# Performance work log

Measured on AMD Instinct MI355X. Metric: run time of the kernel, lower is better.

## Reference

```python
import jax, jax.numpy as jnp
import numpy as np

N_EMBD = 1024

def setup_inputs() -> dict:
    key = jax.random.key(0)
    ks = jax.random.split(key, 7)
    x = jax.random.normal(ks[0], (4, 2048, N_EMBD), dtype=jnp.float32)
    s = 1.0 / np.sqrt(N_EMBD)
    Wk = jax.random.normal(ks[1], (N_EMBD, N_EMBD), dtype=jnp.float32) * s
    bk = jnp.zeros((N_EMBD,), dtype=jnp.float32)
    Wq = jax.random.normal(ks[2], (N_EMBD, N_EMBD), dtype=jnp.float32) * s
    bq = jnp.zeros((N_EMBD,), dtype=jnp.float32)
    Wv = jax.random.normal(ks[3], (N_EMBD, N_EMBD), dtype=jnp.float32) * s
    bv = jnp.zeros((N_EMBD,), dtype=jnp.float32)
    return {"x": x, "Wk": Wk, "bk": bk, "Wq": Wq, "bq": bq, "Wv": Wv, "bv": bv}

def reference(x, Wk, bk, Wq, bq, Wv, bv):
    B, T, C = x.shape
    k = x @ Wk.T + bk  # [B,T,C]
    q = x @ Wq.T + bq
    v = x @ Wv.T + bv
    # scaled scores with causal mask (note: original scales by C**-0.5)
    scores = jnp.einsum('btc,bsc->bts', q, k) * (C ** -0.5)  # [B,T,T]
    causal = jnp.tril(jnp.ones((T, T), dtype=bool))
    scores = jnp.where(causal, scores, -jnp.inf)
    weights = jax.nn.softmax(scores, axis=-1)
    # dropout disabled (inference mode)
    y = jnp.einsum('bts,bsc->btc', weights, v)
    return y
```

## Files before the change

kernel.cpp:

```cpp
#include <hip/hip_runtime.h>
#include <hip/hip_bf16.h>

typedef __attribute__((ext_vector_type(8))) short short8;
typedef __attribute__((ext_vector_type(4))) float f32x4;

__device__ __forceinline__ ushort f2b(float f) {
    __hip_bfloat16 h = __float2bfloat16(f);
    return *reinterpret_cast<ushort*>(&h);
}
__device__ __forceinline__ float b2f(ushort u) {
    return __uint_as_float(((unsigned)u) << 16);
}
__device__ __forceinline__ void gload16(const ushort* g, ushort* l) {
    __builtin_amdgcn_global_load_lds(
        (const __attribute__((address_space(1))) void*)g,
        (__attribute__((address_space(3))) void*)l, 16, 0, 0);
}

__global__ __launch_bounds__(512, 4) void qkv_gemm256(
    const ushort* __restrict__ xb, const ushort* __restrict__ Wcat,
    const float* __restrict__ bk, const float* __restrict__ bq, const float* __restrict__ bv,
    ushort* __restrict__ Kb, ushort* __restrict__ Qb, ushort* __restrict__ Vt) {
    constexpr int T = 2048, C = 1024, K = 1024, NT = 32;
    __shared__ ushort smem[36864];

    const int tid = threadIdx.x;
    const int l = tid & 63, w = tid >> 6;
    const int wm = (w >> 1) * 64, wn = (w & 1) * 64;
    const int lr = l & 15, lk = l >> 4;

    const int b = blockIdx.x;
    const int wg = (b & 7) * 96 + (b >> 3);
    const int m0 = (wg / 24) * 256, n0 = (wg % 24) * 128;

    const int srow = w * 16 + (l >> 2);
    const int scb = ((l & 3) << 4) ^ ((l & 32) ? 32 : 0);
    const ushort* gA = xb + (size_t)(m0 + srow) * K + (scb >> 1);
    const ushort* gB = Wcat + (size_t)(n0 + srow) * K + (scb >> 1);

    const int LB = lr * 32 + ((lk << 3) ^ ((lr >= 8) ? 16 : 0));

    f32x4 acc[4][4] = {};

#define STAGEQ(tt, sl)                                                    \
    {                                                                     \
        const int _ko = (tt) * 32;                                        \
        ushort* _s = smem + (sl) * 12288 + w * 512;                       \
        gload16(gA + _ko,                   _s);                          \
        gload16(gA + (size_t)128 * K + _ko, _s + 4096);                   \
        gload16(gB + _ko,                   _s + 8192);                   \
    }

    STAGEQ(0, 0);
    STAGEQ(1, 1);
    asm volatile("s_waitcnt vmcnt(3)" ::: "memory");
    __builtin_amdgcn_s_barrier();
    asm volatile("" ::: "memory");

    int sc = 0, ss = 2;
    for (int t = 0; t < NT; ++t) {
        const ushort* slot = smem + sc * 12288;
        const ushort* Ab = slot + (wm >> 4) * 512 + LB;
        const ushort* Bb = slot + 8192 + (wn >> 4) * 512 + LB;
        short8 af[4], bf4[4];
#pragma unroll
        for (int f = 0; f < 4; ++f) af[f] = *reinterpret_cast<const short8*>(Ab + f * 512);
#pragma unroll
        for (int g = 0; g < 4; ++g) bf4[g] = *reinterpret_cast<const short8*>(Bb + g * 512);
        if (t + 2 < NT) STAGEQ(t + 2, ss);
        __builtin_amdgcn_s_setprio(1);
#pragma unroll
        for (int f = 0; f < 4; ++f)
#pragma unroll
            for (int g = 0; g < 4; ++g)
                acc[f][g] = __builtin_amdgcn_mfma_f32_16x16x32_bf16(af[f], bf4[g], acc[f][g], 0, 0, 0);
        __builtin_amdgcn_s_setprio(0);
        if (t + 1 < NT) {
            if (t + 2 < NT) asm volatile("s_waitcnt vmcnt(3)" ::: "memory");
            else            asm volatile("s_waitcnt vmcnt(0)" ::: "memory");
            __builtin_amdgcn_s_barrier();
            asm volatile("" ::: "memory");
        }
        sc = (sc == 2) ? 0 : sc + 1;
        ss = (ss == 2) ? 0 : ss + 1;
    }
#undef STAGEQ

    const int zsel = n0 >> 10;
    const int c0 = (n0 & 1023) + wn;
    if (zsel < 2) {
        ushort* O = (zsel == 0) ? Kb : Qb;
        const float* bias = (zsel == 0) ? bk : bq;
#pragma unroll
        for (int f = 0; f < 4; ++f)
#pragma unroll
            for (int g = 0; g < 4; ++g) {
                const int gc = c0 + g * 16 + lr;
                const float badd = bias[gc];
#pragma unroll
                for (int rr = 0; rr < 4; ++rr) {
                    const int gr = m0 + wm + f * 16 + lk * 4 + rr;
                    O[(size_t)gr * C + gc] = f2b(acc[f][g][rr] + badd);
                }
            }
    } else {
        const int zb = (m0 + wm) >> 11;
        const int s0 = (m0 + wm) & 2047;
        ushort* Vz = Vt + (size_t)zb * C * T;
#pragma unroll
        for (int f = 0; f < 4; ++f)
#pragma unroll
            for (int g = 0; g < 4; ++g) {
                const int gc = c0 + g * 16 + lr;
                const float badd = bv[gc];
                const int s = s0 + f * 16 + lk * 4;
                ushort tmp[4];
#pragma unroll
                for (int rr = 0; rr < 4; ++rr) tmp[rr] = f2b(acc[f][g][rr] + badd);
                *reinterpret_cast<uint2*>(Vz + (size_t)gc * T + s) =
                    *reinterpret_cast<uint2*>(tmp);
            }
    }
}

template <int MODE>
__global__ __launch_bounds__(256, 3) void gemm_ring(
    const ushort* __restrict__ Kb, const ushort* __restrict__ Qb,
    const ushort* __restrict__ Vt, ushort* __restrict__ Sb, float* __restrict__ out) {
    constexpr int T = 2048, C = 1024;
    __shared__ ushort smem[24576];

    const int tid = threadIdx.x;
    const int l = tid & 63, w = tid >> 6;
    const int wm = (w >> 1) * 64, wn = (w & 1) * 64;
    const int lr = l & 15, lk = l >> 4;

    int m0, n0, nt, iblk = 0, jblk = 0, z = 0;
    const ushort *Au, *Bu;
    int ldA, ldB;
    if constexpr (MODE == 1) {
        const int wg0 = blockIdx.x;
        const int wg = (wg0 & 7) * 68 + (wg0 >> 3);
        z = wg / 136; const int t136 = wg % 136;
        int i = (int)((sqrtf(8.f * t136 + 1.f) - 1.f) * 0.5f);
        while ((i + 1) * (i + 2) / 2 <= t136) ++i;
        while (i * (i + 1) / 2 > t136) --i;
        const int j = t136 - i * (i + 1) / 2;
        iblk = i; jblk = j;
        m0 = i * 128; n0 = j * 128;
        Au = Qb + (size_t)z * T * C + (size_t)m0 * C; ldA = C;
        Bu = Kb + (size_t)z * T * C + (size_t)n0 * C; ldB = C;
        nt = 32;
    } else {
        const int wg0 = blockIdx.x;
        const int wg = (wg0 & 7) * 64 + (wg0 >> 3);
        const int half = wg >> 8, s2 = wg & 255;
        z = s2 >> 6; const int r6 = s2 & 63;
        const int nb = r6 & 7, ii = r6 >> 3;
        const int i = half ? (15 - ii) : ii;
        iblk = i;
        m0 = i * 128; n0 = nb * 128;
        Au = Sb + (size_t)z * T * T + (size_t)m0 * T; ldA = T;
        Bu = Vt + (size_t)z * C * T + (size_t)n0 * T; ldB = T;
        nt = 4 * (i + 1);
    }

    const int srow = w * 16 + (l >> 2);
    const int scb = ((l & 3) << 4) ^ ((l >= 32) ? 32 : 0);
    const ushort* gA = Au + (size_t)srow * ldA + (scb >> 1);
    const ushort* gB = Bu + (size_t)srow * ldB + (scb >> 1);
    const size_t a64 = (size_t)64 * ldA, b64 = (size_t)64 * ldB;
    const int LBu = lr * 32 + ((lk << 3) ^ ((lr >= 8) ? 16 : 0));

    f32x4 acc[4][4] = {};
    f32x4 acc1[4] = {};
    short8 ones;
#pragma unroll
    for (int q = 0; q < 8; ++q) ones[q] = (short)0x3F80;

#define STAGE(tt, sl)                                                    \
    {                                                                    \
        const int _ko = (tt) * 32;                                       \
        ushort* _d = smem + (sl) * 8192 + w * 512;                       \
        gload16(gA + _ko,        _d);                                    \
        gload16(gA + a64 + _ko,  _d + 2048);                             \
        gload16(gB + _ko,        _d + 4096);                             \
        gload16(gB + b64 + _ko,  _d + 6144);                             \
    }

    STAGE(0, 0);
    STAGE(1, 1);
    asm volatile("s_waitcnt vmcnt(4)" ::: "memory");
    __builtin_amdgcn_s_barrier();
    asm volatile("" ::: "memory");

    int sc = 0, ss = 2;
    for (int t = 0; t < nt; ++t) {
        const ushort* As = smem + sc * 8192 + (wm >> 4) * 512 + LBu;
        const ushort* Bs = smem + sc * 8192 + 4096 + (wn >> 4) * 512 + LBu;
        short8 af[4], bf[4];
#pragma unroll
        for (int q = 0; q < 4; ++q) {
            af[q] = *reinterpret_cast<const short8*>(As + q * 512);
            bf[q] = *reinterpret_cast<const short8*>(Bs + q * 512);
        }
        if (t + 2 < nt) STAGE(t + 2, ss);
        __builtin_amdgcn_s_setprio(1);
#pragma unroll
        for (int mf = 0; mf < 4; ++mf)
#pragma unroll
            for (int nf = 0; nf < 4; ++nf)
                acc[mf][nf] = __builtin_amdgcn_mfma_f32_16x16x32_bf16(af[mf], bf[nf], acc[mf][nf], 0, 0, 0);
        if constexpr (MODE == 2) {
#pragma unroll
            for (int mf = 0; mf < 4; ++mf)
                acc1[mf] = __builtin_amdgcn_mfma_f32_16x16x32_bf16(af[mf], ones, acc1[mf], 0, 0, 0);
        }
        __builtin_amdgcn_s_setprio(0);
        if (t + 1 < nt) {
            if (t + 2 < nt) asm volatile("s_waitcnt vmcnt(4)" ::: "memory");
            else            asm volatile("s_waitcnt vmcnt(0)" ::: "memory");
            __builtin_amdgcn_s_barrier();
            asm volatile("" ::: "memory");
        }
        sc = (sc == 2) ? 0 : sc + 1;
        ss = (ss == 2) ? 0 : ss + 1;
    }
#undef STAGE

    if constexpr (MODE == 1) {
        ushort* Sp = Sb + (size_t)z * T * T;
        const bool diag = (iblk == jblk);
#pragma unroll
        for (int mf = 0; mf < 4; ++mf)
#pragma unroll
            for (int nf = 0; nf < 4; ++nf) {
                const int gc = n0 + wn + nf * 16 + lr;
#pragma unroll
                for (int rr = 0; rr < 4; ++rr) {
                    const int gr = m0 + wm + mf * 16 + lk * 4 + rr;
                    float p = __expf(acc[mf][nf][rr] * 0.03125f);
                    if (diag && gc > gr) p = 0.f;
                    Sp[(size_t)gr * T + gc] = f2b(p);
                }
            }
    } else {
        float* Op = out + (size_t)z * T * C;
#pragma unroll
        for (int mf = 0; mf < 4; ++mf)
#pragma unroll
            for (int rr = 0; rr < 4; ++rr) {
                const int gr = m0 + wm + mf * 16 + lk * 4 + rr;
                const float inv = 1.0f / acc1[mf][rr];
#pragma unroll
                for (int nf = 0; nf < 4; ++nf) {
                    const int gc = n0 + wn + nf * 16 + lr;
                    Op[(size_t)gr * C + gc] = acc[mf][nf][rr] * inv;
                }
            }
    }
}

__global__ __launch_bounds__(256) void cvt_all(
    const float* __restrict__ x, const float* __restrict__ Wk,
    const float* __restrict__ Wq, const float* __restrict__ Wv,
    ushort* __restrict__ xb, ushort* __restrict__ Wcat) {
    constexpr int C = 1024;
    constexpr int NX = 8388608 / 8, NW = C * C / 8;
    int i = blockIdx.x * 256 + threadIdx.x;
    const float* src; ushort* dst;
    if (i < NX)               { src = x;  dst = xb; }
    else if (i < NX + NW)     { src = Wk; dst = Wcat;                 i -= NX; }
    else if (i < NX + 2 * NW) { src = Wq; dst = Wcat + (size_t)C * C; i -= NX + NW; }
    else                      { src = Wv; dst = Wcat + 2 * (size_t)C * C; i -= NX + 2 * NW; }
    const float4* p = reinterpret_cast<const float4*>(src) + (size_t)i * 2;
    float4 a = p[0], b = p[1];
    ushort o[8] = {f2b(a.x), f2b(a.y), f2b(a.z), f2b(a.w),
                   f2b(b.x), f2b(b.y), f2b(b.z), f2b(b.w)};
    reinterpret_cast<uint4*>(dst)[i] = *reinterpret_cast<uint4*>(o);
}

extern "C" void kernel_launch(void* const* d_in, const int* in_sizes, int n_in,
                              void* d_out, int out_size, void* d_ws, size_t ws_size,
                              hipStream_t stream) {
    const float* x  = (const float*)d_in[0];
    const float* Wk = (const float*)d_in[1];
    const float* bk = (const float*)d_in[2];
    const float* Wq = (const float*)d_in[3];
    const float* bq = (const float*)d_in[4];
    const float* Wv = (const float*)d_in[5];
    const float* bv = (const float*)d_in[6];
    float* out = (float*)d_out;

    constexpr int B = 4, T = 2048, C = 1024;
    constexpr size_t BTC = (size_t)B * T * C;

    ushort* Kb = (ushort*)d_ws;
    ushort* Qb = Kb + BTC;
    ushort* Vt = Qb + BTC;
    ushort* Sb = Vt + BTC;
    ushort* xb   = Sb;
    ushort* Wcat = Sb + BTC;

    dim3 blk(256);

    cvt_all<<<dim3(5632), blk, 0, stream>>>(x, Wk, Wq, Wv, xb, Wcat);

    qkv_gemm256<<<dim3(768), dim3(512), 0, stream>>>(xb, Wcat, bk, bq, bv, Kb, Qb, Vt);

    gemm_ring<1><<<dim3(544), blk, 0, stream>>>(Kb, Qb, Vt, Sb, out);

    gemm_ring<2><<<dim3(512), blk, 0, stream>>>(Kb, Qb, Vt, Sb, out);
}
```

Before: 136.8 us.

## Retile QKV GEMM to 128x192 blocks and compute softmax row sums via atomics

The QKV projection GEMM moves from 256x128 tiles on 768 blocks to 128x192 tiles on 1024 blocks, with 8 waves laid out 2x4 at 64x48 each. The epilogue now chooses the K/Q/V destination per 16-column fragment, because a 192-wide tile can straddle the K/Q/V boundaries. Separately, the PV GEMM no longer spends extra MFMAs against a ones vector to get softmax denominators. Instead the score kernel sums the rounded bf16 probabilities per row, reduces them with wave shuffles, and atomically adds them into a rowsum buffer that the conversion kernel zeroes. This adds float atomics and extra workspace, and the load balance changes across the retiled blocks.

```diff
diff --git a/kernel.cpp b/kernel.cpp
--- a/kernel.cpp
+++ b/kernel.cpp
@@ -17,66 +17,72 @@
         (__attribute__((address_space(3))) void*)l, 16, 0, 0);
 }
 
-__global__ __launch_bounds__(512, 4) void qkv_gemm256(
+__global__ __launch_bounds__(512, 4) void qkv_gemm(
     const ushort* __restrict__ xb, const ushort* __restrict__ Wcat,
     const float* __restrict__ bk, const float* __restrict__ bq, const float* __restrict__ bv,
     ushort* __restrict__ Kb, ushort* __restrict__ Qb, ushort* __restrict__ Vt) {
     constexpr int T = 2048, C = 1024, K = 1024, NT = 32;
-    __shared__ ushort smem[36864];
+    __shared__ ushort smem[30720];
 
     const int tid = threadIdx.x;
     const int l = tid & 63, w = tid >> 6;
-    const int wm = (w >> 1) * 64, wn = (w & 1) * 64;
+    const int wm = (w >> 2) * 64, wn = (w & 3) * 48;
     const int lr = l & 15, lk = l >> 4;
 
     const int b = blockIdx.x;
-    const int wg = (b & 7) * 96 + (b >> 3);
-    const int m0 = (wg / 24) * 256, n0 = (wg % 24) * 128;
+    const int wg = (b & 7) * 128 + (b >> 3);
+    const int m0 = (wg >> 4) * 128, n0 = (wg & 15) * 192;
 
     const int srow = w * 16 + (l >> 2);
     const int scb = ((l & 3) << 4) ^ ((l & 32) ? 32 : 0);
-    const ushort* gA = xb + (size_t)(m0 + srow) * K + (scb >> 1);
-    const ushort* gB = Wcat + (size_t)(n0 + srow) * K + (scb >> 1);
+    const ushort* gA  = xb + (size_t)(m0 + srow) * K + (scb >> 1);
+    const ushort* gB  = Wcat + (size_t)(n0 + srow) * K + (scb >> 1);
+    const ushort* gB2 = Wcat + (size_t)(n0 + 128 + srow) * K + (scb >> 1);
 
     const int LB = lr * 32 + ((lk << 3) ^ ((lr >= 8) ? 16 : 0));
 
-    f32x4 acc[4][4] = {};
+    f32x4 acc[4][3] = {};
 
 #define STAGEQ(tt, sl)                                                    \
     {                                                                     \
         const int _ko = (tt) * 32;                                        \
-        ushort* _s = smem + (sl) * 12288 + w * 512;                       \
-        gload16(gA + _ko,                   _s);                          \
-        gload16(gA + (size_t)128 * K + _ko, _s + 4096);                   \
-        gload16(gB + _ko,                   _s + 8192);                   \
+        ushort* _s = smem + (sl) * 10240;                                 \
+        gload16(gA + _ko,  _s + w * 512);                                 \
+        gload16(gB + _ko,  _s + 4096 + w * 512);                          \
+        if (w < 4) gload16(gB2 + _ko, _s + 8192 + w * 512);               \
+    }
+#define WAIT_KEEP1                                                        \
+    {                                                                     \
+        if (w < 4) asm volatile("s_waitcnt vmcnt(3)" ::: "memory");       \
+        else       asm volatile("s_waitcnt vmcnt(2)" ::: "memory");       \
     }
 
     STAGEQ(0, 0);
     STAGEQ(1, 1);
-    asm volatile("s_waitcnt vmcnt(3)" ::: "memory");
+    WAIT_KEEP1;
     __builtin_amdgcn_s_barrier();
     asm volatile("" ::: "memory");
 
     int sc = 0, ss = 2;
     for (int t = 0; t < NT; ++t) {
-        const ushort* slot = smem + sc * 12288;
+        const ushort* slot = smem + sc * 10240;
         const ushort* Ab = slot + (wm >> 4) * 512 + LB;
-        const ushort* Bb = slot + 8192 + (wn >> 4) * 512 + LB;
-        short8 af[4], bf4[4];
+        const ushort* Bb = slot + 4096 + (wn >> 4) * 512 + LB;
+        short8 af[4], bf3[3];
 #pragma unroll
         for (int f = 0; f < 4; ++f) af[f] = *reinterpret_cast<const short8*>(Ab + f * 512);
 #pragma unroll
-        for (int g = 0; g < 4; ++g) bf4[g] = *reinterpret_cast<const short8*>(Bb + g * 512);
+        for (int g = 0; g < 3; ++g) bf3[g] = *reinterpret_cast<const short8*>(Bb + g * 512);
         if (t + 2 < NT) STAGEQ(t + 2, ss);
         __builtin_amdgcn_s_setprio(1);
 #pragma unroll
         for (int f = 0; f < 4; ++f)
 #pragma unroll
-            for (int g = 0; g < 4; ++g)
-                acc[f][g] = __builtin_amdgcn_mfma_f32_16x16x32_bf16(af[f], bf4[g], acc[f][g], 0, 0, 0);
+            for (int g = 0; g < 3; ++g)
+                acc[f][g] = __builtin_amdgcn_mfma_f32_16x16x32_bf16(af[f], bf3[g], acc[f][g], 0, 0, 0);
         __builtin_amdgcn_s_setprio(0);
         if (t + 1 < NT) {
-            if (t + 2 < NT) asm volatile("s_waitcnt vmcnt(3)" ::: "memory");
+            if (t + 2 < NT) { WAIT_KEEP1; }
             else            asm volatile("s_waitcnt vmcnt(0)" ::: "memory");
             __builtin_amdgcn_s_barrier();
             asm volatile("" ::: "memory");
@@ -85,48 +91,46 @@
         ss = (ss == 2) ? 0 : ss + 1;
     }
 #undef STAGEQ
-
-    const int zsel = n0 >> 10;
-    const int c0 = (n0 & 1023) + wn;
-    if (zsel < 2) {
-        ushort* O = (zsel == 0) ? Kb : Qb;
-        const float* bias = (zsel == 0) ? bk : bq;
-#pragma unroll
-        for (int f = 0; f < 4; ++f)
-#pragma unroll
-            for (int g = 0; g < 4; ++g) {
-                const int gc = c0 + g * 16 + lr;
-                const float badd = bias[gc];
+#undef WAIT_KEEP1
+
+    const int zb = (m0 + wm) >> 11;
+    const int s0 = (m0 + wm) & 2047;
+    ushort* Vz = Vt + (size_t)zb * C * T;
+#pragma unroll
+    for (int g = 0; g < 3; ++g) {
+        const int nbase = n0 + wn + g * 16;
+        const int zf = nbase >> 10;
+        const int cf = (nbase & 1023) + lr;
+        if (zf < 2) {
+            ushort* O = (zf == 0) ? Kb : Qb;
+            const float badd = ((zf == 0) ? bk : bq)[cf];
+#pragma unroll
+            for (int f = 0; f < 4; ++f)
 #pragma unroll
                 for (int rr = 0; rr < 4; ++rr) {
                     const int gr = m0 + wm + f * 16 + lk * 4 + rr;
-                    O[(size_t)gr * C + gc] = f2b(acc[f][g][rr] + badd);
+                    O[(size_t)gr * C + cf] = f2b(acc[f][g][rr] + badd);
                 }
-            }
-    } else {
-        const int zb = (m0 + wm) >> 11;
-        const int s0 = (m0 + wm) & 2047;
-        ushort* Vz = Vt + (size_t)zb * C * T;
-#pragma unroll
-        for (int f = 0; f < 4; ++f)
-#pragma unroll
-            for (int g = 0; g < 4; ++g) {
-                const int gc = c0 + g * 16 + lr;
-                const float badd = bv[gc];
+        } else {
+            const float badd = bv[cf];
+#pragma unroll
+            for (int f = 0; f < 4; ++f) {
                 const int s = s0 + f * 16 + lk * 4;
                 ushort tmp[4];
 #pragma unroll
                 for (int rr = 0; rr < 4; ++rr) tmp[rr] = f2b(acc[f][g][rr] + badd);
-                *reinterpret_cast<uint2*>(Vz + (size_t)gc * T + s) =
+                *reinterpret_cast<uint2*>(Vz + (size_t)cf * T + s) =
                     *reinterpret_cast<uint2*>(tmp);
             }
+        }
     }
 }
 
 template <int MODE>
 __global__ __launch_bounds__(256, 3) void gemm_ring(
     const ushort* __restrict__ Kb, const ushort* __restrict__ Qb,
-    const ushort* __restrict__ Vt, ushort* __restrict__ Sb, float* __restrict__ out) {
+    const ushort* __restrict__ Vt, ushort* __restrict__ Sb,
+    float* __restrict__ rowsum, float* __restrict__ out) {
     constexpr int T = 2048, C = 1024;
     __shared__ ushort smem[24576];
 
@@ -173,10 +177,6 @@
     const int LBu = lr * 32 + ((lk << 3) ^ ((lr >= 8) ? 16 : 0));
 
     f32x4 acc[4][4] = {};
-    f32x4 acc1[4] = {};
-    short8 ones;
-#pragma unroll
-    for (int q = 0; q < 8; ++q) ones[q] = (short)0x3F80;
 
 #define STAGE(tt, sl)                                                    \
     {                                                                    \
@@ -211,11 +211,6 @@
 #pragma unroll
             for (int nf = 0; nf < 4; ++nf)
                 acc[mf][nf] = __builtin_amdgcn_mfma_f32_16x16x32_bf16(af[mf], bf[nf], acc[mf][nf], 0, 0, 0);
-        if constexpr (MODE == 2) {
-#pragma unroll
-            for (int mf = 0; mf < 4; ++mf)
-                acc1[mf] = __builtin_amdgcn_mfma_f32_16x16x32_bf16(af[mf], ones, acc1[mf], 0, 0, 0);
-        }
         __builtin_amdgcn_s_setprio(0);
         if (t + 1 < nt) {
             if (t + 2 < nt) asm volatile("s_waitcnt vmcnt(4)" ::: "memory");
@@ -231,6 +226,11 @@
     if constexpr (MODE == 1) {
         ushort* Sp = Sb + (size_t)z * T * T;
         const bool diag = (iblk == jblk);
+        float rp[4][4];
+#pragma unroll
+        for (int mf = 0; mf < 4; ++mf)
+#pragma unroll
+            for (int rr = 0; rr < 4; ++rr) rp[mf][rr] = 0.f;
 #pragma unroll
         for (int mf = 0; mf < 4; ++mf)
 #pragma unroll
@@ -241,17 +241,34 @@
                     const int gr = m0 + wm + mf * 16 + lk * 4 + rr;
                     float p = __expf(acc[mf][nf][rr] * 0.03125f);
                     if (diag && gc > gr) p = 0.f;
-                    Sp[(size_t)gr * T + gc] = f2b(p);
+                    const ushort us = f2b(p);
+                    Sp[(size_t)gr * T + gc] = us;
+                    rp[mf][rr] += b2f(us);
+                }
+            }
+#pragma unroll
+        for (int mf = 0; mf < 4; ++mf)
+#pragma unroll
+            for (int rr = 0; rr < 4; ++rr) {
+                float v = rp[mf][rr];
+                v += __shfl_xor(v, 1);
+                v += __shfl_xor(v, 2);
+                v += __shfl_xor(v, 4);
+                v += __shfl_xor(v, 8);
+                if (lr == 0) {
+                    const int gr = m0 + wm + mf * 16 + lk * 4 + rr;
+                    atomicAdd(&rowsum[(size_t)z * T + gr], v);
                 }
             }
     } else {
         float* Op = out + (size_t)z * T * C;
+        const float* rs = rowsum + (size_t)z * T;
 #pragma unroll
         for (int mf = 0; mf < 4; ++mf)
 #pragma unroll
             for (int rr = 0; rr < 4; ++rr) {
                 const int gr = m0 + wm + mf * 16 + lk * 4 + rr;
-                const float inv = 1.0f / acc1[mf][rr];
+                const float inv = 1.0f / rs[gr];
 #pragma unroll
                 for (int nf = 0; nf < 4; ++nf) {
                     const int gc = n0 + wn + nf * 16 + lr;
@@ -264,9 +281,16 @@
 __global__ __launch_bounds__(256) void cvt_all(
     const float* __restrict__ x, const float* __restrict__ Wk,
     const float* __restrict__ Wq, const float* __restrict__ Wv,
-    ushort* __restrict__ xb, ushort* __restrict__ Wcat) {
+    ushort* __restrict__ xb, ushort* __restrict__ Wcat,
+    float* __restrict__ rowsum) {
     constexpr int C = 1024;
     constexpr int NX = 8388608 / 8, NW = C * C / 8;
+    if (blockIdx.x >= 5632) {
+        const int idx = (blockIdx.x - 5632) * 256 + threadIdx.x;
+        float4 zz = {0.f, 0.f, 0.f, 0.f};
+        reinterpret_cast<float4*>(rowsum)[idx] = zz;
+        return;
+    }
     int i = blockIdx.x * 256 + threadIdx.x;
     const float* src; ushort* dst;
     if (i < NX)               { src = x;  dst = xb; }
@@ -299,16 +323,17 @@
     ushort* Qb = Kb + BTC;
     ushort* Vt = Qb + BTC;
     ushort* Sb = Vt + BTC;
+    float* rowsum = (float*)(Sb + (size_t)B * T * T);
     ushort* xb   = Sb;
     ushort* Wcat = Sb + BTC;
 
     dim3 blk(256);
 
-    cvt_all<<<dim3(5632), blk, 0, stream>>>(x, Wk, Wq, Wv, xb, Wcat);
-
-    qkv_gemm256<<<dim3(768), dim3(512), 0, stream>>>(xb, Wcat, bk, bq, bv, Kb, Qb, Vt);
-
-    gemm_ring<1><<<dim3(544), blk, 0, stream>>>(Kb, Qb, Vt, Sb, out);
-
-    gemm_ring<2><<<dim3(512), blk, 0, stream>>>(Kb, Qb, Vt, Sb, out);
-}
+    cvt_all<<<dim3(5640), blk, 0, stream>>>(x, Wk, Wq, Wv, xb, Wcat, rowsum);
+
+    qkv_gemm<<<dim3(1024), dim3(512), 0, stream>>>(xb, Wcat, bk, bq, bv, Kb, Qb, Vt);
+
+    gemm_ring<1><<<dim3(544), blk, 0, stream>>>(Kb, Qb, Vt, Sb, rowsum, out);
+
+    gemm_ring<2><<<dim3(512), blk, 0, stream>>>(Kb, Qb, Vt, Sb, rowsum, out);
+}
```

Result: slower. 143.8 us (+5.1%).
